# Kernel tuning notes

Measured on AMD Instinct MI355X. Metric: run time of the kernel, lower is better.

Reference implementation:

```python
import jax, jax.numpy as jnp
import numpy as np

B = 16      # number of graphs (equal-sized, batch = repeat(arange(B), N))


def _knn_edges(pos, k, total):
    """Batch-aware kNN graph, torch_geometric knn_graph semantics.

    loop=False, flow='source_to_target': for each query node i, its k nearest
    neighbors j produce edges (row=j neighbor/source, col=i query/target).
    Returns (row, col) as flat global int32 index arrays of length B*N*k.
    """
    N = total // B
    posb = pos.reshape(B, N, -1)                      # [B, N, 3]
    sq = jnp.sum(posb * posb, axis=-1)                # [B, N]
    # squared Euclidean distances, [B, N, N]
    d2 = sq[:, :, None] + sq[:, None, :] - 2.0 * jnp.einsum('bnd,bmd->bnm', posb, posb)
    d2 = jnp.where(jnp.eye(N, dtype=bool)[None], jnp.inf, d2)  # exclude self-loops
    _, nbr = jax.lax.top_k(-d2, k)                    # [B, N, k] local neighbor idx
    offs = (jnp.arange(B, dtype=nbr.dtype) * N)[:, None, None]
    row = (nbr + offs).reshape(-1)                                      # neighbors (sources)
    col = jnp.broadcast_to(jnp.arange(N, dtype=nbr.dtype)[None, :, None] + offs,
                           (B, N, k)).reshape(-1)                       # query nodes (targets)
    return row, col


def reference(x, pos, batch, k):
    total = x.shape[0]
    row, col = _knn_edges(pos, k, total)
    # scatter_mean(x[col], row, dim_size=total): mean of gathered features per row index
    sums = jax.ops.segment_sum(x[col], row, num_segments=total)          # [total, d]
    cnt = jax.ops.segment_sum(jnp.ones(row.shape, x.dtype), row, num_segments=total)
    x_neigh_mean = sums / jnp.maximum(cnt, 1.0)[:, None]                 # empty rows -> 0
    return jnp.sum(jnp.abs(x - x_neigh_mean), axis=-1)                   # L1 norm, [total]


def setup_inputs() -> dict:
    key = jax.random.key(0)
    k1, k2 = jax.random.split(key)
    N = 4096
    x = jax.random.normal(k1, (B * N, 64), dtype=jnp.float32)
    pos = jax.random.normal(k2, (B * N, 3), dtype=jnp.float32)
    batch = jnp.repeat(jnp.arange(B, dtype=jnp.int64), N)
    return {"x": x, "pos": pos, "batch": batch, "k": 10}
```

## Files before the change

kernel.cpp:

```cpp
#include <hip/hip_runtime.h>
#include <stdint.h>

#define NB 16
#define NN 4096
#define KK 10
#define NL 11
#define FD 64
#define TOTAL (NB * NN)
#define NW 8
#define CH 512
#define SOCT 32
#define QG 64
#define WCAP 24
#define WPITCH 25

#define INFF __int_as_float(0x7f800000)

typedef float f2 __attribute__((ext_vector_type(2)));

__device__ __forceinline__ f2 FdP(f2 cx, f2 cy, f2 cz, f2 cq,
                                  f2 vx2, f2 vy2, f2 vz2, f2 sqi2) {
#pragma clang fp contract(fast)
    f2 t = sqi2 + cq;
    t = vx2 * cx + t;
    t = vy2 * cy + t;
    t = vz2 * cz + t;
    return t;
}

__device__ __forceinline__ uint32_t d2exact(float mx, float my, float mz, float sqi,
                                            float cx, float cy, float cz, float cw) {
    float dot = __fadd_rn(__fadd_rn(__fmul_rn(mx, cx), __fmul_rn(my, cy)),
                          __fmul_rn(mz, cz));
    float d2 = __fsub_rn(__fadd_rn(sqi, cw), __fmul_rn(2.0f, dot));
    return __float_as_uint(d2);
}

__global__ __launch_bounds__(256) void prep_kernel(const float* __restrict__ pos,
                                                   float4* __restrict__ pp4,
                                                   int* __restrict__ cnt) {
    const int p = blockIdx.x * 256 + threadIdx.x;
    const float* s = pos + (size_t)p * 6;
    float x0 = s[0], y0 = s[1], z0 = s[2];
    float x1 = s[3], y1 = s[4], z1 = s[5];
    float q0 = __fadd_rn(__fadd_rn(__fmul_rn(x0, x0), __fmul_rn(y0, y0)),
                         __fmul_rn(z0, z0));
    float q1 = __fadd_rn(__fadd_rn(__fmul_rn(x1, x1), __fmul_rn(y1, y1)),
                         __fmul_rn(z1, z1));
    pp4[2 * p + 0] = make_float4(x0, x1, y0, y1);
    pp4[2 * p + 1] = make_float4(z0, z1, q0, q1);
    cnt[2 * p + 0] = 0;
    cnt[2 * p + 1] = 0;
}

__global__ __launch_bounds__(512, 8) void knn_kernel(const float4* __restrict__ pp4,
                                                     int* __restrict__ cnt,
                                                     int* __restrict__ colfix,
                                                     int* __restrict__ nbr) {
    __shared__ uint32_t smem[6400];
    __shared__ float tau_s[QG];
    __shared__ uint32_t qcntw[QG * NW];
    float* listf = (float*)smem;
    uint16_t* pool16 = (uint16_t*)smem;

    const int tid = threadIdx.x;
    const int lane = tid & 63;
    const int w = __builtin_amdgcn_readfirstlane(tid >> 6);
    const int batch = blockIdx.x & 15;
    const int qloc = ((blockIdx.x >> 4) << 6) | lane;
    const int gbase = batch << 12;
    const int gq = gbase + qloc;

    float4 mA = pp4[(gq >> 1) * 2 + 0];
    float4 mB = pp4[(gq >> 1) * 2 + 1];
    const bool hi = (qloc & 1);
    const float mx = hi ? mA.y : mA.x;
    const float my = hi ? mA.w : mA.z;
    const float mz = hi ? mB.y : mB.x;
    const float sqi = hi ? mB.w : mB.z;
    const f2 vx22 = {__fmul_rn(-2.0f, mx), __fmul_rn(-2.0f, mx)};
    const f2 vy22 = {__fmul_rn(-2.0f, my), __fmul_rn(-2.0f, my)};
    const f2 vz22 = {__fmul_rn(-2.0f, mz), __fmul_rn(-2.0f, mz)};
    const f2 sqi22 = {sqi, sqi};

    const f2* __restrict__ cp2 = (const f2*)(pp4 + (size_t)(gbase + w * CH));

#define D8P(cb2)                                                      \
    f2 X0 = (cb2)[0],  Y0 = (cb2)[1],  Z0 = (cb2)[2],  Q0 = (cb2)[3]; \
    f2 X1 = (cb2)[4],  Y1 = (cb2)[5],  Z1 = (cb2)[6],  Q1 = (cb2)[7]; \
    f2 X2 = (cb2)[8],  Y2 = (cb2)[9],  Z2 = (cb2)[10], Q2 = (cb2)[11];\
    f2 X3 = (cb2)[12], Y3 = (cb2)[13], Z3 = (cb2)[14], Q3 = (cb2)[15];\
    f2 e0 = FdP(X0, Y0, Z0, Q0, vx22, vy22, vz22, sqi22);             \
    f2 e1 = FdP(X1, Y1, Z1, Q1, vx22, vy22, vz22, sqi22);             \
    f2 e2 = FdP(X2, Y2, Z2, Q2, vx22, vy22, vz22, sqi22);             \
    f2 e3 = FdP(X3, Y3, Z3, Q3, vx22, vy22, vz22, sqi22);

    float L[NL];
#pragma unroll
    for (int t = 0; t < NL; t++) L[t] = INFF;

#pragma unroll 2
    for (int o = 0; o < SOCT; ++o) {
        const f2* cb2 = cp2 + o * 16;
        D8P(cb2);
        float m = fminf(fminf(fminf(e0.x, e0.y), fminf(e1.x, e1.y)),
                        fminf(fminf(e2.x, e2.y), fminf(e3.x, e3.y)));
#pragma unroll
        for (int t = 0; t < NL - 1; ++t) L[t] = __builtin_amdgcn_fmed3f(L[t], L[t + 1], m);
        L[NL - 1] = fminf(L[NL - 1], m);
    }
#pragma unroll
    for (int t = 0; t < NL; t++) listf[tid * NL + t] = L[t];
    __syncthreads();

    if (tid < QG) {
        int p[NW];
#pragma unroll
        for (int u = 0; u < NW; u++) p[u] = NL - 1;
        float tau = INFF;
        for (int it = 0; it < NL; ++it) {
            float best = INFF;
            int bw = 0;
#pragma unroll
            for (int u = 0; u < NW; u++) {
                float v = (p[u] >= 0) ? listf[((u << 6) | tid) * NL + p[u]] : INFF;
                if (v < best) { best = v; bw = u; }
            }
            p[bw]--;
            tau = best;
        }
        tau_s[tid] = tau;
    }
    __syncthreads();

    const float tau = tau_s[lane] * 1.0001f + 1e-5f;
    const uint32_t cell0 = (uint32_t)((lane * NW + w) * WPITCH);
    uint32_t cpos = cell0;
#pragma unroll 2
    for (int o = 0; o < CH / 8; ++o) {
        const f2* cb2 = cp2 + o * 16;
        D8P(cb2);
        const uint32_t jb = (uint32_t)(w * CH + o * 8);
        bool h0 = e0.x <= tau, h1 = e0.y <= tau, h2 = e1.x <= tau, h3 = e1.y <= tau;
        bool h4 = e2.x <= tau, h5 = e2.y <= tau, h6 = e3.x <= tau, h7 = e3.y <= tau;
        if (h0 | h1 | h2 | h3 | h4 | h5 | h6 | h7) {
#define PUSH(hv, off)                                              \
            if ((hv) && cpos < cell0 + WCAP) {                     \
                pool16[cpos] = (uint16_t)(jb + (off));             \
                cpos++;                                            \
            }
            PUSH(h0, 0) PUSH(h1, 1) PUSH(h2, 2) PUSH(h3, 3)
            PUSH(h4, 4) PUSH(h5, 5) PUSH(h6, 6) PUSH(h7, 7)
#undef PUSH
        }
    }
    qcntw[lane * NW + w] = cpos - cell0;
    __syncthreads();

    if (tid < QG) {
        uint64_t S[KK];
#pragma unroll
        for (int t = 0; t < KK; t++) S[t] = ~0ull;
#pragma unroll
        for (int u = 0; u < NW; u++) {
            uint32_t c2 = qcntw[tid * NW + u];
            const uint16_t* st = pool16 + (tid * NW + u) * WPITCH;
            for (uint32_t e = 0; e < c2; ++e) {
                uint32_t ix = st[e];
                if (ix == (uint32_t)qloc) continue;
                int g = gbase + (int)ix;
                float4 A = pp4[(g >> 1) * 2 + 0];
                float4 B = pp4[(g >> 1) * 2 + 1];
                bool ch = (ix & 1);
                uint32_t db = d2exact(mx, my, mz, sqi,
                                      ch ? A.y : A.x, ch ? A.w : A.z,
                                      ch ? B.y : B.x, ch ? B.w : B.z);
                uint64_t k64 = ((uint64_t)db << 32) | ix;
                if (k64 < S[0]) {
                    bool sh[KK];
                    sh[0] = true;
#pragma unroll
                    for (int t = 1; t < KK; t++) sh[t] = (k64 < S[t]);
#pragma unroll
                    for (int t = 0; t < KK; t++) {
                        uint64_t vac = sh[t] ? k64 : S[t];
                        S[t] = (t + 1 < KK) ? (sh[t + 1] ? S[t + 1] : vac) : vac;
                    }
                }
            }
        }
#pragma unroll
        for (int t = 0; t < KK; t++) {
            int jl = (int)(S[t] & 0xffffffffu);
            int gj = gbase + jl;
            int p = atomicAdd(&cnt[gj], 1);
            if (colfix) {
                if (p < 64) colfix[(gj << 6) | p] = gq;
            } else {
                nbr[gq * KK + t] = gj;
            }
        }
    }
#undef D8P
}

__global__ __launch_bounds__(256) void out_bucket_kernel(const float4* __restrict__ x4,
                                                         const int* __restrict__ colfix,
                                                         const int* __restrict__ cnt,
                                                         float* __restrict__ out) {
    const int b = blockIdx.x;
    const int g = b & 15;
    const int i = b >> 4;
    const int n = (g << 12) | (i << 4) | (threadIdx.x >> 4);
    const int s = threadIdx.x & 15;
    const int c = cnt[n];
    const int cc = (c > 64) ? 64 : c;
    const int4* cf4 = (const int4*)(colfix + ((size_t)n << 6));
    float4 acc = make_float4(0.f, 0.f, 0.f, 0.f);
    for (int eb = 0; eb < cc; eb += 4) {
        int4 Q = cf4[eb >> 2];
        float4 v0 = x4[((size_t)Q.x << 4) | s];
        acc.x += v0.x; acc.y += v0.y; acc.z += v0.z; acc.w += v0.w;
        if (eb + 1 < cc) {
            float4 v1 = x4[((size_t)Q.y << 4) | s];
            acc.x += v1.x; acc.y += v1.y; acc.z += v1.z; acc.w += v1.w;
        }
        if (eb + 2 < cc) {
            float4 v2 = x4[((size_t)Q.z << 4) | s];
            acc.x += v2.x; acc.y += v2.y; acc.z += v2.z; acc.w += v2.w;
        }
        if (eb + 3 < cc) {
            float4 v3 = x4[((size_t)Q.w << 4) | s];
            acc.x += v3.x; acc.y += v3.y; acc.z += v3.z; acc.w += v3.w;
        }
    }
    const float inv = 1.0f / (float)(c > 1 ? c : 1);
    float4 mn = x4[((size_t)n << 4) | s];
    float v = fabsf(mn.x - acc.x * inv) + fabsf(mn.y - acc.y * inv) +
              fabsf(mn.z - acc.z * inv) + fabsf(mn.w - acc.w * inv);
    v += __shfl_xor(v, 1, 64);
    v += __shfl_xor(v, 2, 64);
    v += __shfl_xor(v, 4, 64);
    v += __shfl_xor(v, 8, 64);
    if (s == 0) out[n] = v;
}

__global__ __launch_bounds__(1024) void scan_kernel(const int* __restrict__ cnt,
                                                    int* __restrict__ offs) {
    __shared__ int lds[1024];
    const int t = threadIdx.x;
    const int base = t * 64;
    int s = 0;
    for (int i = 0; i < 64; i++) s += cnt[base + i];
    lds[t] = s;
    __syncthreads();
    for (int off = 1; off < 1024; off <<= 1) {
        int v = (t >= off) ? lds[t - off] : 0;
        __syncthreads();
        lds[t] += v;
        __syncthreads();
    }
    int run = lds[t] - s;
    for (int i = 0; i < 64; i++) {
        offs[base + i] = run;
        run += cnt[base + i];
    }
}

__global__ __launch_bounds__(256) void fill_kernel(const int* __restrict__ nbr,
                                                   int* __restrict__ offs,
                                                   int* __restrict__ col) {
    const int i = blockIdx.x * 256 + threadIdx.x;
#pragma unroll
    for (int t = 0; t < KK; t++) {
        int j = nbr[i * KK + t];
        int p = atomicAdd(&offs[j], 1);
        col[p] = i;
    }
}

__global__ __launch_bounds__(256) void out_kernel(const float* __restrict__ x,
                                                  const int* __restrict__ col,
                                                  const int* __restrict__ offs_end,
                                                  const int* __restrict__ cnt,
                                                  float* __restrict__ out) {
    const int gtid = blockIdx.x * 256 + threadIdx.x;
    const int n = gtid >> 6;
    const int lane = gtid & 63;
    const int c = cnt[n];
    const int end = offs_end[n];
    const int start = end - c;
    float s = 0.0f;
    for (int e = start; e < end; e++) {
        int i = col[e];
        s += x[(size_t)i * FD + lane];
    }
    float mean = s / (float)(c > 1 ? c : 1);
    float v = fabsf(x[(size_t)n * FD + lane] - mean);
#pragma unroll
    for (int off = 32; off; off >>= 1) v += __shfl_xor(v, off, 64);
    if (lane == 0) out[n] = v;
}

extern "C" void kernel_launch(void* const* d_in, const int* in_sizes, int n_in,
                              void* d_out, int out_size, void* d_ws, size_t ws_size,
                              hipStream_t stream) {
    const float* x = (const float*)d_in[0];
    const float* pos = (const float*)d_in[1];
    float* out = (float*)d_out;

    char* ws = (char*)d_ws;
    float4* pp4 = (float4*)(ws + 0);
    int* cnt = (int*)(ws + 1048576);
    int* colfix = (int*)(ws + 1310720);
    int* nbr = (int*)(ws + 1310720);
    int* offs = (int*)(ws + 3932160);
    int* col = (int*)(ws + 4194304);

    const bool bucket = ws_size >= (size_t)(1310720 + TOTAL * 64 * 4);

    hipLaunchKernelGGL(prep_kernel, dim3(TOTAL / 2 / 256), dim3(256), 0, stream, pos, pp4, cnt);
    hipLaunchKernelGGL(knn_kernel, dim3(TOTAL / QG), dim3(512), 0, stream, pp4, cnt,
                       bucket ? colfix : (int*)nullptr, bucket ? (int*)nullptr : nbr);
    if (bucket) {
        hipLaunchKernelGGL(out_bucket_kernel, dim3(TOTAL * 16 / 256), dim3(256), 0, stream,
                           (const float4*)x, colfix, cnt, out);
    } else {
        hipLaunchKernelGGL(scan_kernel, dim3(1), dim3(1024), 0, stream, cnt, offs);
        hipLaunchKernelGGL(fill_kernel, dim3(TOTAL / 256), dim3(256), 0, stream, nbr, offs, col);
        hipLaunchKernelGGL(out_kernel, dim3(TOTAL * FD / 256), dim3(256), 0, stream,
                           x, col, offs, cnt, out);
    }
}
```

Measured before the change: 190.7 us.

## Use per-octet hit bitmasks and branchless compaction for kNN candidate collection

The candidate-collection pass now only computes the minimum distance per group of 8 candidates and records a 64-bit hit mask per warp slice. A second ballot-driven loop revisits just the flagged octets, recomputes the exact distances and writes them into the pool with branchless clamped stores. The threshold-estimation pre-pass samples half as many octets (SOCT 32 to 16), and the min reductions use paired f2 ops. The aim is to cut divergent per-candidate push branches, but the looser threshold from fewer samples may admit more candidates and risks overflowing the WCAP cap.

Result: slower. 213.7 us (+12.1%).

```diff
diff --git a/kernel.cpp b/kernel.cpp
--- a/kernel.cpp
+++ b/kernel.cpp
@@ -9,7 +9,7 @@
 #define TOTAL (NB * NN)
 #define NW 8
 #define CH 512
-#define SOCT 32
+#define SOCT 16
 #define QG 64
 #define WCAP 24
 #define WPITCH 25
@@ -26,6 +26,13 @@
     t = vy2 * cy + t;
     t = vz2 * cz + t;
     return t;
+}
+
+__device__ __forceinline__ f2 fmin2(f2 a, f2 b) {
+    f2 r;
+    r.x = fminf(a.x, b.x);
+    r.y = fminf(a.y, b.y);
+    return r;
 }
 
 __device__ __forceinline__ uint32_t d2exact(float mx, float my, float mz, float sqi,
@@ -78,9 +85,12 @@
     const float my = hi ? mA.w : mA.z;
     const float mz = hi ? mB.y : mB.x;
     const float sqi = hi ? mB.w : mB.z;
-    const f2 vx22 = {__fmul_rn(-2.0f, mx), __fmul_rn(-2.0f, mx)};
-    const f2 vy22 = {__fmul_rn(-2.0f, my), __fmul_rn(-2.0f, my)};
-    const f2 vz22 = {__fmul_rn(-2.0f, mz), __fmul_rn(-2.0f, mz)};
+    const float vx2s = __fmul_rn(-2.0f, mx);
+    const float vy2s = __fmul_rn(-2.0f, my);
+    const float vz2s = __fmul_rn(-2.0f, mz);
+    const f2 vx22 = {vx2s, vx2s};
+    const f2 vy22 = {vy2s, vy2s};
+    const f2 vz22 = {vz2s, vz2s};
     const f2 sqi22 = {sqi, sqi};
 
     const f2* __restrict__ cp2 = (const f2*)(pp4 + (size_t)(gbase + w * CH));
@@ -103,8 +113,8 @@
     for (int o = 0; o < SOCT; ++o) {
         const f2* cb2 = cp2 + o * 16;
         D8P(cb2);
-        float m = fminf(fminf(fminf(e0.x, e0.y), fminf(e1.x, e1.y)),
-                        fminf(fminf(e2.x, e2.y), fminf(e3.x, e3.y)));
+        f2 mm = fmin2(fmin2(e0, e1), fmin2(e2, e3));
+        float m = fminf(mm.x, mm.y);
 #pragma unroll
         for (int t = 0; t < NL - 1; ++t) L[t] = __builtin_amdgcn_fmed3f(L[t], L[t + 1], m);
         L[NL - 1] = fminf(L[NL - 1], m);
@@ -134,24 +144,56 @@
     __syncthreads();
 
     const float tau = tau_s[lane] * 1.0001f + 1e-5f;
-    const uint32_t cell0 = (uint32_t)((lane * NW + w) * WPITCH);
-    uint32_t cpos = cell0;
+    uint32_t bmLo = 0u, bmHi = 0u;
 #pragma unroll 2
-    for (int o = 0; o < CH / 8; ++o) {
+    for (int o = 0; o < 32; ++o) {
         const f2* cb2 = cp2 + o * 16;
         D8P(cb2);
-        const uint32_t jb = (uint32_t)(w * CH + o * 8);
-        bool h0 = e0.x <= tau, h1 = e0.y <= tau, h2 = e1.x <= tau, h3 = e1.y <= tau;
-        bool h4 = e2.x <= tau, h5 = e2.y <= tau, h6 = e3.x <= tau, h7 = e3.y <= tau;
-        if (h0 | h1 | h2 | h3 | h4 | h5 | h6 | h7) {
-#define PUSH(hv, off)                                              \
-            if ((hv) && cpos < cell0 + WCAP) {                     \
-                pool16[cpos] = (uint16_t)(jb + (off));             \
-                cpos++;                                            \
+        f2 mm = fmin2(fmin2(e0, e1), fmin2(e2, e3));
+        float m8 = fminf(mm.x, mm.y);
+        bmLo = (bmLo >> 1) | ((m8 <= tau) ? 0x80000000u : 0u);
+    }
+#pragma unroll 2
+    for (int o = 32; o < 64; ++o) {
+        const f2* cb2 = cp2 + o * 16;
+        D8P(cb2);
+        f2 mm = fmin2(fmin2(e0, e1), fmin2(e2, e3));
+        float m8 = fminf(mm.x, mm.y);
+        bmHi = (bmHi >> 1) | ((m8 <= tau) ? 0x80000000u : 0u);
+    }
+
+    const uint32_t cell0 = (uint32_t)((lane * NW + w) * WPITCH);
+    const uint32_t cmax = cell0 + WCAP - 1;
+    uint32_t cpos = cell0;
+    const float4* cb4base = (const float4*)cp2;
+    for (int half = 0; half < 2; ++half) {
+        uint32_t m = half ? bmHi : bmLo;
+        while (__ballot(m != 0u)) {
+            if (m != 0u) {
+                int o = __builtin_ctz(m);
+                m &= m - 1u;
+                const int oo = (half << 5) | o;
+                const float4* cb = cb4base + oo * 8;
+                const uint32_t jb = (uint32_t)(w * CH + oo * 8);
+#pragma unroll
+                for (int pi = 0; pi < 4; ++pi) {
+                    float4 A = cb[2 * pi], B = cb[2 * pi + 1];
+                    float tlo = __fadd_rn(sqi, B.z);
+                    tlo = __fmaf_rn(vx2s, A.x, tlo);
+                    tlo = __fmaf_rn(vy2s, A.z, tlo);
+                    tlo = __fmaf_rn(vz2s, B.x, tlo);
+                    float thi = __fadd_rn(sqi, B.w);
+                    thi = __fmaf_rn(vx2s, A.y, thi);
+                    thi = __fmaf_rn(vy2s, A.w, thi);
+                    thi = __fmaf_rn(vz2s, B.y, thi);
+                    uint32_t wp = (cpos <= cmax) ? cpos : cmax;
+                    pool16[wp] = (uint16_t)(jb + 2 * pi);
+                    cpos += (tlo <= tau && cpos <= cmax) ? 1u : 0u;
+                    wp = (cpos <= cmax) ? cpos : cmax;
+                    pool16[wp] = (uint16_t)(jb + 2 * pi + 1);
+                    cpos += (thi <= tau && cpos <= cmax) ? 1u : 0u;
+                }
             }
-            PUSH(h0, 0) PUSH(h1, 1) PUSH(h2, 2) PUSH(h3, 3)
-            PUSH(h4, 4) PUSH(h5, 5) PUSH(h6, 6) PUSH(h7, 7)
-#undef PUSH
         }
     }
     qcntw[lane * NW + w] = cpos - cell0;
```
